# Optimization experiments

Hardware: AMD Instinct MI355X
Metric: run time of the kernel (lower is better)

Reference implementation:

```python
import jax, jax.numpy as jnp
import numpy as np

EMBED_DIM = 1024
NUM_HEADS = 16
NUM_KV_HEADS = 4
HEAD_DIM = EMBED_DIM // NUM_HEADS  # 64
N_GROUP = NUM_HEADS // NUM_KV_HEADS  # 4
KV_DIM = NUM_KV_HEADS * HEAD_DIM  # 256


def setup_inputs() -> dict:
    key = jax.random.key(0)
    ks = jax.random.split(key, 9)
    B, T = 1, 4096
    s_in = 1.0 / np.sqrt(EMBED_DIM)
    inp = {
        "x": jax.random.normal(ks[0], (B, T, EMBED_DIM), dtype=jnp.float32),
        "Wq": jax.random.normal(ks[1], (EMBED_DIM, EMBED_DIM), dtype=jnp.float32) * s_in,
        "bq": jnp.zeros((EMBED_DIM,), dtype=jnp.float32),
        "Wk": jax.random.normal(ks[2], (KV_DIM, EMBED_DIM), dtype=jnp.float32) * s_in,
        "bk": jnp.zeros((KV_DIM,), dtype=jnp.float32),
        "Wv": jax.random.normal(ks[3], (KV_DIM, EMBED_DIM), dtype=jnp.float32) * s_in,
        "bv": jnp.zeros((KV_DIM,), dtype=jnp.float32),
        "Wo": jax.random.normal(ks[4], (EMBED_DIM, EMBED_DIM), dtype=jnp.float32) * s_in,
        "bo": jnp.zeros((EMBED_DIM,), dtype=jnp.float32),
    }
    return inp


def reference(x, Wq, bq, Wk, bk, Wv, bv, Wo, bo):
    B, T, C = x.shape
    scale = HEAD_DIM ** -0.5
    # projections (torch Linear: x @ W.T + b)
    Q = x @ Wq.T + bq  # [B,T,C]
    K = x @ Wk.T + bk  # [B,T,KV_DIM]
    V = x @ Wv.T + bv
    Q = Q.reshape(B, T, NUM_HEADS, HEAD_DIM).transpose(0, 2, 1, 3)      # [B,H,T,D]
    K = K.reshape(B, T, NUM_KV_HEADS, HEAD_DIM).transpose(0, 2, 1, 3)   # [B,Hkv,T,D]
    V = V.reshape(B, T, NUM_KV_HEADS, HEAD_DIM).transpose(0, 2, 1, 3)
    new_kv = (K, V)
    # GQA: group Q heads over KV heads instead of materializing repeated K/V
    Qg = Q.reshape(B, NUM_KV_HEADS, N_GROUP, T, HEAD_DIM)  # head h uses kv head h//N_GROUP
    scores = jnp.einsum('bkgqd,bkvd->bkgqv', Qg, K) * scale  # [B,Hkv,G,T,T]
    weights = jax.nn.softmax(scores, axis=-1)
    out = jnp.einsum('bkgqv,bkvd->bkgqd', weights, V)  # [B,Hkv,G,T,D]
    out = out.reshape(B, NUM_HEADS, T, HEAD_DIM).transpose(0, 2, 1, 3).reshape(B, T, C)
    output = out @ Wo.T + bo
    return (output, new_kv)
```

## Files before the change

### kernel.cpp

```cpp
#include <hip/hip_runtime.h>
#include <hip/hip_bf16.h>
#include <math.h>

typedef unsigned short u16;
typedef __bf16 bf16;
typedef __bf16 bf16x8 __attribute__((ext_vector_type(8)));
typedef float f32x4 __attribute__((ext_vector_type(4)));
typedef u16 u16x4 __attribute__((ext_vector_type(4)));
typedef u16 u16x8 __attribute__((ext_vector_type(8)));

#define QSCALE 0.1803368801111204f

static __device__ __forceinline__ u16 f2b(float f) {
  return __builtin_bit_cast(u16, (bf16)f);
}

static __device__ __forceinline__ f32x4 mfma16(u16x8 a, u16x8 b, f32x4 c) {
  return __builtin_amdgcn_mfma_f32_16x16x32_bf16(
      __builtin_bit_cast(bf16x8, a), __builtin_bit_cast(bf16x8, b), c, 0, 0, 0);
}

static __device__ __forceinline__ void glds16(const u16* g, u16* l) {
  __builtin_amdgcn_global_load_lds(
      (const __attribute__((address_space(1))) void*)g,
      (__attribute__((address_space(3))) void*)l, 16, 0, 0);
}

#define WAIT_VM0() asm volatile("s_waitcnt vmcnt(0)" ::: "memory")

static __device__ __forceinline__ u16x8 ldsrd(const u16* base, int row, int slot) {
  return *(const u16x8*)(base + row * 64 + ((slot ^ (row & 7)) * 8));
}

__global__ void cast_f32_bf16(const float* __restrict__ src, u16* __restrict__ dst, int n4) {
  int i = blockIdx.x * blockDim.x + threadIdx.x;
  int stride = gridDim.x * blockDim.x;
  for (; i < n4; i += stride) {
    f32x4 v = ((const f32x4*)src)[i];
    u16x4 o;
#pragma unroll
    for (int r = 0; r < 4; r++) o[r] = f2b(v[r]);
    ((u16x4*)dst)[i] = o;
  }
}

template<int MODE>
__global__ __launch_bounds__(256, 2) void gemm_bt(
    const u16* __restrict__ A, const u16* __restrict__ B,
    const float* __restrict__ b0, const float* __restrict__ b1,
    const float* __restrict__ b2,
    float* __restrict__ outF,
    u16* __restrict__ qs, u16* __restrict__ kb, u16* __restrict__ vt,
    int K) {
  __shared__ u16 As[2][128 * 64];
  __shared__ u16 Bs[2][128 * 64];
  const int t = threadIdx.x, w = t >> 6, l = t & 63;
  const int c = l & 15, g = l >> 4;
  const int n0 = blockIdx.x * 128, m0 = blockIdx.y * 128;
  const int nrow0 = (w >> 1) * 64, mrow0 = (w & 1) * 64;
  const int srow = l >> 3, sslot = l & 7;

  f32x4 acc[4][4];
  f32x4 z = {0.f, 0.f, 0.f, 0.f};
#pragma unroll
  for (int i = 0; i < 4; i++)
#pragma unroll
    for (int j = 0; j < 4; j++) acc[i][j] = z;

#pragma unroll
  for (int p = 0; p < 4; p++) {
    int row = p * 32 + w * 8 + srow;
    int ss = sslot ^ (row & 7);
    glds16(A + (size_t)(m0 + row) * K + ss * 8, &As[0][p * 2048 + w * 512]);
    glds16(B + (size_t)(n0 + row) * K + ss * 8, &Bs[0][p * 2048 + w * 512]);
  }
  WAIT_VM0();
  __builtin_amdgcn_s_barrier();

  const int NS = K >> 6;
  for (int st = 0; st < NS; ++st) {
    const int cur = st & 1;
    if (st + 1 < NS) {
      int kt = (st + 1) * 64;
#pragma unroll
      for (int p = 0; p < 4; p++) {
        int row = p * 32 + w * 8 + srow;
        int ss = sslot ^ (row & 7);
        glds16(A + (size_t)(m0 + row) * K + kt + ss * 8, &As[cur ^ 1][p * 2048 + w * 512]);
        glds16(B + (size_t)(n0 + row) * K + kt + ss * 8, &Bs[cur ^ 1][p * 2048 + w * 512]);
      }
    }
    __builtin_amdgcn_s_setprio(1);
#pragma unroll
    for (int ks = 0; ks < 2; ks++) {
      u16x8 af[4], bf[4];
#pragma unroll
      for (int nj = 0; nj < 4; nj++) af[nj] = ldsrd(Bs[cur], nrow0 + 16 * nj + c, g + 4 * ks);
#pragma unroll
      for (int mi = 0; mi < 4; mi++) bf[mi] = ldsrd(As[cur], mrow0 + 16 * mi + c, g + 4 * ks);
#pragma unroll
      for (int nj = 0; nj < 4; nj++)
#pragma unroll
        for (int mi = 0; mi < 4; mi++) acc[nj][mi] = mfma16(af[nj], bf[mi], acc[nj][mi]);
    }
    __builtin_amdgcn_s_setprio(0);
    WAIT_VM0();
    __builtin_amdgcn_s_barrier();
  }

#pragma unroll
  for (int nj = 0; nj < 4; nj++) {
#pragma unroll
    for (int mi = 0; mi < 4; mi++) {
      int n = n0 + nrow0 + 16 * nj + 4 * g;
      int m = m0 + mrow0 + 16 * mi + c;
      f32x4 v = acc[nj][mi];
      if (MODE == 1) {
        f32x4 bb = *(const f32x4*)(b0 + n);
        v += bb;
        *(f32x4*)(outF + (size_t)m * 1024 + n) = v;
      } else {
        if (n < 1024) {
          f32x4 bb = *(const f32x4*)(b0 + n);
          v += bb;
          u16x4 q;
#pragma unroll
          for (int r = 0; r < 4; r++) q[r] = f2b(v[r] * QSCALE);
          *(u16x4*)(qs + (size_t)m * 1024 + n) = q;
        } else if (n < 1280) {
          int nn = n - 1024, khh = nn >> 6, d = nn & 63;
          f32x4 bb = *(const f32x4*)(b1 + nn);
          v += bb;
          *(f32x4*)(outF + (size_t)4194304 + (size_t)(khh * 4096 + m) * 64 + d) = v;
          u16x4 kq;
#pragma unroll
          for (int r = 0; r < 4; r++) kq[r] = f2b(v[r]);
          *(u16x4*)(kb + (size_t)(khh * 4096 + m) * 64 + d) = kq;
        } else {
          int nn = n - 1280, khh = nn >> 6, d = nn & 63;
          f32x4 bb = *(const f32x4*)(b2 + nn);
          v += bb;
          *(f32x4*)(outF + (size_t)5242880 + (size_t)(khh * 4096 + m) * 64 + d) = v;
#pragma unroll
          for (int r = 0; r < 4; r++) vt[(size_t)(khh * 64 + d + r) * 4096 + m] = f2b(v[r]);
        }
      }
    }
  }
}

__global__ __launch_bounds__(256, 4) void attn_fwd(
    const u16* __restrict__ qs, const u16* __restrict__ kb,
    const u16* __restrict__ vt, u16* __restrict__ att) {
  __shared__ u16 Ks[2][64 * 64];
  __shared__ u16 Vs[2][64 * 64];
  __shared__ u16 Ps[4][16 * 64];
  const int h = blockIdx.y, kh = h >> 2;
  const int q0 = blockIdx.x * 64;
  const int t = threadIdx.x, w = t >> 6, l = t & 63;
  const int c = l & 15, g = l >> 4;
  const int srow = l >> 3, sslot = l & 7;

  const u16* kbase = kb + (size_t)kh * 4096 * 64;
  const u16* vbase = vt + (size_t)kh * 64 * 4096;

  u16x8 qf[2];
#pragma unroll
  for (int ks = 0; ks < 2; ks++)
    qf[ks] = *(const u16x8*)(qs + (size_t)(q0 + w * 16 + c) * 1024 + h * 64 + g * 8 + ks * 32);

  f32x4 o[4];
  f32x4 z = {0.f, 0.f, 0.f, 0.f};
#pragma unroll
  for (int dj = 0; dj < 4; dj++) o[dj] = z;
  float m_r = -INFINITY, l_r = 0.f;

#pragma unroll
  for (int p = 0; p < 2; p++) {
    int row = p * 32 + w * 8 + srow;
    int ss = sslot ^ (row & 7);
    glds16(kbase + (size_t)row * 64 + ss * 8, &Ks[0][p * 2048 + w * 512]);
    glds16(vbase + (size_t)row * 4096 + ss * 8, &Vs[0][p * 2048 + w * 512]);
  }
  WAIT_VM0();
  __builtin_amdgcn_s_barrier();

  for (int tt = 0; tt < 64; ++tt) {
    const int cur = tt & 1;
    const u16* KsC = Ks[cur];
    const u16* VsC = Vs[cur];
    if (tt < 63) {
      int kv = (tt + 1) * 64;
#pragma unroll
      for (int p = 0; p < 2; p++) {
        int row = p * 32 + w * 8 + srow;
        int ss = sslot ^ (row & 7);
        glds16(kbase + (size_t)(kv + row) * 64 + ss * 8, &Ks[cur ^ 1][p * 2048 + w * 512]);
        glds16(vbase + (size_t)row * 4096 + kv + ss * 8, &Vs[cur ^ 1][p * 2048 + w * 512]);
      }
    }

    f32x4 s[4];
#pragma unroll
    for (int kj = 0; kj < 4; kj++) s[kj] = z;
    __builtin_amdgcn_s_setprio(1);
#pragma unroll
    for (int ks = 0; ks < 2; ks++) {
      u16x8 kf[4];
#pragma unroll
      for (int kj = 0; kj < 4; kj++) kf[kj] = ldsrd(KsC, 16 * kj + c, g + 4 * ks);
#pragma unroll
      for (int kj = 0; kj < 4; kj++) s[kj] = mfma16(kf[kj], qf[ks], s[kj]);
    }
    __builtin_amdgcn_s_setprio(0);

    float pm = fmaxf(fmaxf(fmaxf(s[0][0], s[0][1]), fmaxf(s[0][2], s[0][3])),
                     fmaxf(fmaxf(s[1][0], s[1][1]), fmaxf(s[1][2], s[1][3])));
    pm = fmaxf(pm, fmaxf(fmaxf(fmaxf(s[2][0], s[2][1]), fmaxf(s[2][2], s[2][3])),
                         fmaxf(fmaxf(s[3][0], s[3][1]), fmaxf(s[3][2], s[3][3]))));
    pm = fmaxf(pm, __shfl_xor(pm, 16));
    pm = fmaxf(pm, __shfl_xor(pm, 32));
    float fac = 1.f;
    if (!__all(pm - m_r <= 8.0f)) {
      float mn = fmaxf(m_r, pm);
      fac = __builtin_amdgcn_exp2f(m_r - mn);
      m_r = mn;
#pragma unroll
      for (int dj = 0; dj < 4; dj++) o[dj] *= fac;
    }
    float ls = 0.f;
#pragma unroll
    for (int kj = 0; kj < 4; kj++) {
      u16x4 pk;
#pragma unroll
      for (int r = 0; r < 4; r++) {
        float p = __builtin_amdgcn_exp2f(s[kj][r] - m_r);
        ls += p;
        pk[r] = f2b(p);
      }
      int sl = (2 * kj + (g >> 1)) ^ (c & 7);
      *(u16x4*)(&Ps[w][c * 64 + sl * 8 + (g & 1) * 4]) = pk;
    }
    ls += __shfl_xor(ls, 16);
    ls += __shfl_xor(ls, 32);
    l_r = l_r * fac + ls;

    __builtin_amdgcn_s_setprio(1);
#pragma unroll
    for (int ks = 0; ks < 2; ks++) {
      u16x8 vf[4], pf;
#pragma unroll
      for (int dj = 0; dj < 4; dj++) vf[dj] = ldsrd(VsC, 16 * dj + c, g + 4 * ks);
      pf = ldsrd(Ps[w], c, g + 4 * ks);
#pragma unroll
      for (int dj = 0; dj < 4; dj++) o[dj] = mfma16(vf[dj], pf, o[dj]);
    }
    __builtin_amdgcn_s_setprio(0);

    WAIT_VM0();
    __builtin_amdgcn_s_barrier();
  }

  float inv = 1.f / l_r;
#pragma unroll
  for (int dj = 0; dj < 4; dj++) {
    u16x4 ov;
#pragma unroll
    for (int r = 0; r < 4; r++) ov[r] = f2b(o[dj][r] * inv);
    *(u16x4*)(att + (size_t)(q0 + w * 16 + c) * 1024 + h * 64 + 16 * dj + 4 * g) = ov;
  }
}

extern "C" void kernel_launch(void* const* d_in, const int* in_sizes, int n_in,
                              void* d_out, int out_size, void* d_ws, size_t ws_size,
                              hipStream_t stream) {
  const float* x  = (const float*)d_in[0];
  const float* Wq = (const float*)d_in[1];
  const float* bq = (const float*)d_in[2];
  const float* Wk = (const float*)d_in[3];
  const float* bk = (const float*)d_in[4];
  const float* Wv = (const float*)d_in[5];
  const float* bv = (const float*)d_in[6];
  const float* Wo = (const float*)d_in[7];
  const float* bo = (const float*)d_in[8];
  float* out = (float*)d_out;
  char* ws = (char*)d_ws;

  u16* X16  = (u16*)(ws);
  u16* WQKV = (u16*)(ws + 8388608);
  u16* WO16 = (u16*)(ws + 11534336);
  u16* QS   = (u16*)(ws + 13631488);
  u16* KB   = (u16*)(ws + 22020096);
  u16* VT   = (u16*)(ws + 24117248);
  u16* ATT  = X16;

  cast_f32_bf16<<<1024, 256, 0, stream>>>(x, X16, 4096 * 1024 / 4);
  cast_f32_bf16<<<256, 256, 0, stream>>>(Wq, WQKV, 1024 * 1024 / 4);
  cast_f32_bf16<<<64, 256, 0, stream>>>(Wk, WQKV + 1024 * 1024, 256 * 1024 / 4);
  cast_f32_bf16<<<64, 256, 0, stream>>>(Wv, WQKV + 1280 * 1024, 256 * 1024 / 4);
  cast_f32_bf16<<<256, 256, 0, stream>>>(Wo, WO16, 1024 * 1024 / 4);

  gemm_bt<0><<<dim3(12, 32), 256, 0, stream>>>(X16, WQKV, bq, bk, bv, out, QS, KB, VT, 1024);
  attn_fwd<<<dim3(64, 16), 256, 0, stream>>>(QS, KB, VT, ATT);
  gemm_bt<1><<<dim3(8, 32), 256, 0, stream>>>(ATT, WO16, bo, nullptr, nullptr, out,
                                              nullptr, nullptr, nullptr, 1024);
}
```

Baseline: 260.6 us.

## Use 32x32 MFMA attention with register-resident P and separate V transpose

Attention now uses 32x32x16 bf16 MFMAs with 128 queries per block and 32 per wave. P stays in registers, rearranged with v_permlane32_swap instead of a round trip through LDS, and the row sum is computed by an MFMA against a ones vector. The strided scattered V-transpose stores in the QKV GEMM epilogue become contiguous stores plus a dedicated LDS-tiled transpose kernel. The four weight cast launches are merged into one. The changes cut LDS traffic, shuffles and launch overhead, at the cost of lower occupancy (launch bounds 4 to 2), an extra kernel, and VT reusing the WQKV workspace region.

```diff
diff --git a/kernel.cpp b/kernel.cpp
--- a/kernel.cpp
+++ b/kernel.cpp
@@ -3,21 +3,37 @@
 #include <math.h>
 
 typedef unsigned short u16;
+typedef unsigned int u32;
 typedef __bf16 bf16;
 typedef __bf16 bf16x8 __attribute__((ext_vector_type(8)));
 typedef float f32x4 __attribute__((ext_vector_type(4)));
+typedef float f32x16 __attribute__((ext_vector_type(16)));
+typedef u16 u16x2 __attribute__((ext_vector_type(2)));
 typedef u16 u16x4 __attribute__((ext_vector_type(4)));
 typedef u16 u16x8 __attribute__((ext_vector_type(8)));
+typedef u32 u32x4 __attribute__((ext_vector_type(4)));
 
 #define QSCALE 0.1803368801111204f
 
 static __device__ __forceinline__ u16 f2b(float f) {
   return __builtin_bit_cast(u16, (bf16)f);
+}
+static __device__ __forceinline__ u32 pack2(float a, float b) {
+  u16x2 p = { f2b(a), f2b(b) };
+  return __builtin_bit_cast(u32, p);
 }
 
 static __device__ __forceinline__ f32x4 mfma16(u16x8 a, u16x8 b, f32x4 c) {
   return __builtin_amdgcn_mfma_f32_16x16x32_bf16(
       __builtin_bit_cast(bf16x8, a), __builtin_bit_cast(bf16x8, b), c, 0, 0, 0);
+}
+static __device__ __forceinline__ f32x16 mfma32(u16x8 a, u16x8 b, f32x16 c) {
+  return __builtin_amdgcn_mfma_f32_32x32x16_bf16(
+      __builtin_bit_cast(bf16x8, a), __builtin_bit_cast(bf16x8, b), c, 0, 0, 0);
+}
+
+static __device__ __forceinline__ void pl32swap(u32& a, u32& b) {
+  asm("v_permlane32_swap_b32 %0, %1" : "+v"(a), "+v"(b));
 }
 
 static __device__ __forceinline__ void glds16(const u16* g, u16* l) {
@@ -44,13 +60,53 @@
   }
 }
 
+__global__ void cast_weights(const float* __restrict__ Wq, const float* __restrict__ Wk,
+                             const float* __restrict__ Wv, const float* __restrict__ Wo,
+                             u16* __restrict__ wqkv, u16* __restrict__ wo16) {
+  int i = blockIdx.x * blockDim.x + threadIdx.x;
+  int stride = gridDim.x * blockDim.x;
+  for (; i < 655360; i += stride) {
+    const float* src; u16* dst; int j;
+    if (i < 262144)      { src = Wq; dst = wqkv;           j = i; }
+    else if (i < 327680) { src = Wk; dst = wqkv + 1048576; j = i - 262144; }
+    else if (i < 393216) { src = Wv; dst = wqkv + 1310720; j = i - 327680; }
+    else                 { src = Wo; dst = wo16;           j = i - 393216; }
+    f32x4 v = ((const f32x4*)src)[j];
+    u16x4 o;
+#pragma unroll
+    for (int r = 0; r < 4; r++) o[r] = f2b(v[r]);
+    ((u16x4*)dst)[j] = o;
+  }
+}
+
+__global__ void transpose_v(const u16* __restrict__ vb, u16* __restrict__ vt) {
+  __shared__ u16 T[64][72];
+  const int kh = blockIdx.y;
+  const int t0 = blockIdx.x * 64;
+  const int tid = threadIdx.x;
+  const int r = tid >> 2, c0 = (tid & 3) * 16;
+  const u16* src = vb + ((size_t)kh * 4096 + t0 + r) * 64 + c0;
+  *(u16x8*)&T[r][c0] = *(const u16x8*)src;
+  *(u16x8*)&T[r][c0 + 8] = *(const u16x8*)(src + 8);
+  __syncthreads();
+  const int d = tid >> 2, j0 = (tid & 3) * 16;
+  u16x8 o0, o1;
+#pragma unroll
+  for (int j = 0; j < 8; j++) o0[j] = T[j0 + j][d];
+#pragma unroll
+  for (int j = 0; j < 8; j++) o1[j] = T[j0 + 8 + j][d];
+  u16* dst = vt + ((size_t)kh * 64 + d) * 4096 + t0 + j0;
+  *(u16x8*)dst = o0;
+  *(u16x8*)(dst + 8) = o1;
+}
+
 template<int MODE>
 __global__ __launch_bounds__(256, 2) void gemm_bt(
     const u16* __restrict__ A, const u16* __restrict__ B,
     const float* __restrict__ b0, const float* __restrict__ b1,
     const float* __restrict__ b2,
     float* __restrict__ outF,
-    u16* __restrict__ qs, u16* __restrict__ kb, u16* __restrict__ vt,
+    u16* __restrict__ qs, u16* __restrict__ kb, u16* __restrict__ vb,
     int K) {
   __shared__ u16 As[2][128 * 64];
   __shared__ u16 Bs[2][128 * 64];
@@ -141,39 +197,43 @@
           f32x4 bb = *(const f32x4*)(b2 + nn);
           v += bb;
           *(f32x4*)(outF + (size_t)5242880 + (size_t)(khh * 4096 + m) * 64 + d) = v;
-#pragma unroll
-          for (int r = 0; r < 4; r++) vt[(size_t)(khh * 64 + d + r) * 4096 + m] = f2b(v[r]);
+          u16x4 vq;
+#pragma unroll
+          for (int r = 0; r < 4; r++) vq[r] = f2b(v[r]);
+          *(u16x4*)(vb + (size_t)(khh * 4096 + m) * 64 + d) = vq;
         }
       }
     }
   }
 }
 
-__global__ __launch_bounds__(256, 4) void attn_fwd(
+__global__ __launch_bounds__(256, 2) void attn_fwd(
     const u16* __restrict__ qs, const u16* __restrict__ kb,
     const u16* __restrict__ vt, u16* __restrict__ att) {
   __shared__ u16 Ks[2][64 * 64];
   __shared__ u16 Vs[2][64 * 64];
-  __shared__ u16 Ps[4][16 * 64];
   const int h = blockIdx.y, kh = h >> 2;
-  const int q0 = blockIdx.x * 64;
+  const int q0 = blockIdx.x * 128;
   const int t = threadIdx.x, w = t >> 6, l = t & 63;
-  const int c = l & 15, g = l >> 4;
+  const int ql = l & 31, hh = l >> 5;
   const int srow = l >> 3, sslot = l & 7;
 
-  const u16* kbase = kb + (size_t)kh * 4096 * 64;
-  const u16* vbase = vt + (size_t)kh * 64 * 4096;
-
-  u16x8 qf[2];
-#pragma unroll
-  for (int ks = 0; ks < 2; ks++)
-    qf[ks] = *(const u16x8*)(qs + (size_t)(q0 + w * 16 + c) * 1024 + h * 64 + g * 8 + ks * 32);
-
-  f32x4 o[4];
-  f32x4 z = {0.f, 0.f, 0.f, 0.f};
-#pragma unroll
-  for (int dj = 0; dj < 4; dj++) o[dj] = z;
-  float m_r = -INFINITY, l_r = 0.f;
+  const u16* kbase = kb + (size_t)kh * 262144;
+  const u16* vbase = vt + (size_t)kh * 262144;
+
+  u16x8 qf[4];
+#pragma unroll
+  for (int ks = 0; ks < 4; ks++)
+    qf[ks] = *(const u16x8*)(qs + (size_t)(q0 + w * 32 + ql) * 1024 + h * 64 + ks * 16 + hh * 8);
+
+  u16x8 onesf;
+#pragma unroll
+  for (int j = 0; j < 8; j++) onesf[j] = 0x3F80;
+
+  f32x16 o0v, o1v, lacc;
+#pragma unroll
+  for (int i = 0; i < 16; i++) { o0v[i] = 0.f; o1v[i] = 0.f; lacc[i] = 0.f; }
+  float m_r = -INFINITY;
 
 #pragma unroll
   for (int p = 0; p < 2; p++) {
@@ -200,60 +260,61 @@
       }
     }
 
-    f32x4 s[4];
-#pragma unroll
-    for (int kj = 0; kj < 4; kj++) s[kj] = z;
+    f32x16 sA, sB;
+#pragma unroll
+    for (int i = 0; i < 16; i++) { sA[i] = 0.f; sB[i] = 0.f; }
     __builtin_amdgcn_s_setprio(1);
 #pragma unroll
-    for (int ks = 0; ks < 2; ks++) {
-      u16x8 kf[4];
-#pragma unroll
-      for (int kj = 0; kj < 4; kj++) kf[kj] = ldsrd(KsC, 16 * kj + c, g + 4 * ks);
-#pragma unroll
-      for (int kj = 0; kj < 4; kj++) s[kj] = mfma16(kf[kj], qf[ks], s[kj]);
+    for (int ks = 0; ks < 4; ks++) {
+      u16x8 kf0 = ldsrd(KsC, ql, 2 * ks + hh);
+      u16x8 kf1 = ldsrd(KsC, 32 + ql, 2 * ks + hh);
+      sA = mfma32(kf0, qf[ks], sA);
+      sB = mfma32(kf1, qf[ks], sB);
     }
     __builtin_amdgcn_s_setprio(0);
 
-    float pm = fmaxf(fmaxf(fmaxf(s[0][0], s[0][1]), fmaxf(s[0][2], s[0][3])),
-                     fmaxf(fmaxf(s[1][0], s[1][1]), fmaxf(s[1][2], s[1][3])));
-    pm = fmaxf(pm, fmaxf(fmaxf(fmaxf(s[2][0], s[2][1]), fmaxf(s[2][2], s[2][3])),
-                         fmaxf(fmaxf(s[3][0], s[3][1]), fmaxf(s[3][2], s[3][3]))));
-    pm = fmaxf(pm, __shfl_xor(pm, 16));
-    pm = fmaxf(pm, __shfl_xor(pm, 32));
-    float fac = 1.f;
+    float mx[16];
+#pragma unroll
+    for (int i = 0; i < 16; i++) mx[i] = fmaxf(sA[i], sB[i]);
+#pragma unroll
+    for (int stp = 8; stp > 0; stp >>= 1)
+#pragma unroll
+      for (int i = 0; i < stp; i++) mx[i] = fmaxf(mx[i], mx[i + stp]);
+    float pm = fmaxf(mx[0], __shfl_xor(mx[0], 32));
+
     if (!__all(pm - m_r <= 8.0f)) {
       float mn = fmaxf(m_r, pm);
-      fac = __builtin_amdgcn_exp2f(m_r - mn);
+      float fac = __builtin_amdgcn_exp2f(m_r - mn);
       m_r = mn;
-#pragma unroll
-      for (int dj = 0; dj < 4; dj++) o[dj] *= fac;
-    }
-    float ls = 0.f;
-#pragma unroll
-    for (int kj = 0; kj < 4; kj++) {
-      u16x4 pk;
-#pragma unroll
-      for (int r = 0; r < 4; r++) {
-        float p = __builtin_amdgcn_exp2f(s[kj][r] - m_r);
-        ls += p;
-        pk[r] = f2b(p);
-      }
-      int sl = (2 * kj + (g >> 1)) ^ (c & 7);
-      *(u16x4*)(&Ps[w][c * 64 + sl * 8 + (g & 1) * 4]) = pk;
-    }
-    ls += __shfl_xor(ls, 16);
-    ls += __shfl_xor(ls, 32);
-    l_r = l_r * fac + ls;
+      o0v *= fac; o1v *= fac; lacc *= fac;
+    }
+
+    u32 pw0[8], pw1[8];
+#pragma unroll
+    for (int i = 0; i < 8; i++) {
+      pw0[i] = pack2(__builtin_amdgcn_exp2f(sA[2 * i] - m_r),
+                     __builtin_amdgcn_exp2f(sA[2 * i + 1] - m_r));
+      pw1[i] = pack2(__builtin_amdgcn_exp2f(sB[2 * i] - m_r),
+                     __builtin_amdgcn_exp2f(sB[2 * i + 1] - m_r));
+    }
 
     __builtin_amdgcn_s_setprio(1);
 #pragma unroll
-    for (int ks = 0; ks < 2; ks++) {
-      u16x8 vf[4], pf;
-#pragma unroll
-      for (int dj = 0; dj < 4; dj++) vf[dj] = ldsrd(VsC, 16 * dj + c, g + 4 * ks);
-      pf = ldsrd(Ps[w], c, g + 4 * ks);
-#pragma unroll
-      for (int dj = 0; dj < 4; dj++) o[dj] = mfma16(vf[dj], pf, o[dj]);
+    for (int t4 = 0; t4 < 4; t4++) {
+      u32 a0, a1, b0, b1;
+      if (t4 == 0)      { a0 = pw0[0]; a1 = pw0[1]; b0 = pw0[2]; b1 = pw0[3]; }
+      else if (t4 == 1) { a0 = pw0[4]; a1 = pw0[5]; b0 = pw0[6]; b1 = pw0[7]; }
+      else if (t4 == 2) { a0 = pw1[0]; a1 = pw1[1]; b0 = pw1[2]; b1 = pw1[3]; }
+      else              { a0 = pw1[4]; a1 = pw1[5]; b0 = pw1[6]; b1 = pw1[7]; }
+      pl32swap(a0, b0);
+      pl32swap(a1, b1);
+      u32x4 pv4 = {a0, a1, b0, b1};
+      u16x8 pf = __builtin_bit_cast(u16x8, pv4);
+      u16x8 vf0 = ldsrd(VsC, ql, 2 * t4 + hh);
+      u16x8 vf1 = ldsrd(VsC, 32 + ql, 2 * t4 + hh);
+      o0v = mfma32(vf0, pf, o0v);
+      o1v = mfma32(vf1, pf, o1v);
+      lacc = mfma32(onesf, pf, lacc);
     }
     __builtin_amdgcn_s_setprio(0);
 
@@ -261,14 +322,18 @@
     __builtin_amdgcn_s_barrier();
   }
 
-  float inv = 1.f / l_r;
-#pragma unroll
-  for (int dj = 0; dj < 4; dj++) {
-    u16x4 ov;
-#pragma unroll
-    for (int r = 0; r < 4; r++) ov[r] = f2b(o[dj][r] * inv);
-    *(u16x4*)(att + (size_t)(q0 + w * 16 + c) * 1024 + h * 64 + 16 * dj + 4 * g) = ov;
-  }
+  float inv = 1.f / lacc[0];
+  const size_t obase = (size_t)(q0 + w * 32 + ql) * 1024 + h * 64;
+#pragma unroll
+  for (int dj = 0; dj < 2; dj++)
+#pragma unroll
+    for (int rq = 0; rq < 4; rq++) {
+      u16x4 ov;
+#pragma unroll
+      for (int r = 0; r < 4; r++)
+        ov[r] = f2b((dj ? o1v[rq * 4 + r] : o0v[rq * 4 + r]) * inv);
+      *(u16x4*)(att + obase + dj * 32 + rq * 8 + hh * 4) = ov;
+    }
 }
 
 extern "C" void kernel_launch(void* const* d_in, const int* in_sizes, int n_in,
@@ -288,20 +353,19 @@
 
   u16* X16  = (u16*)(ws);
   u16* WQKV = (u16*)(ws + 8388608);
+  u16* VT   = (u16*)(ws + 8388608);
   u16* WO16 = (u16*)(ws + 11534336);
   u16* QS   = (u16*)(ws + 13631488);
   u16* KB   = (u16*)(ws + 22020096);
-  u16* VT   = (u16*)(ws + 24117248);
+  u16* VB   = (u16*)(ws + 24117248);
   u16* ATT  = X16;
 
   cast_f32_bf16<<<1024, 256, 0, stream>>>(x, X16, 4096 * 1024 / 4);
-  cast_f32_bf16<<<256, 256, 0, stream>>>(Wq, WQKV, 1024 * 1024 / 4);
-  cast_f32_bf16<<<64, 256, 0, stream>>>(Wk, WQKV + 1024 * 1024, 256 * 1024 / 4);
-  cast_f32_bf16<<<64, 256, 0, stream>>>(Wv, WQKV + 1280 * 1024, 256 * 1024 / 4);
-  cast_f32_bf16<<<256, 256, 0, stream>>>(Wo, WO16, 1024 * 1024 / 4);
-
-  gemm_bt<0><<<dim3(12, 32), 256, 0, stream>>>(X16, WQKV, bq, bk, bv, out, QS, KB, VT, 1024);
-  attn_fwd<<<dim3(64, 16), 256, 0, stream>>>(QS, KB, VT, ATT);
+  cast_weights<<<512, 256, 0, stream>>>(Wq, Wk, Wv, Wo, WQKV, WO16);
+
+  gemm_bt<0><<<dim3(12, 32), 256, 0, stream>>>(X16, WQKV, bq, bk, bv, out, QS, KB, VB, 1024);
+  transpose_v<<<dim3(64, 4), 256, 0, stream>>>(VB, VT);
+  attn_fwd<<<dim3(32, 16), 256, 0, stream>>>(QS, KB, VT, ATT);
   gemm_bt<1><<<dim3(8, 32), 256, 0, stream>>>(ATT, WO16, bo, nullptr, nullptr, out,
                                               nullptr, nullptr, nullptr, 1024);
 }
```

After: 241.2 us. -7.5%, faster.
